# Kernel optimization log

Measured on AMD Instinct MI355X. Metric: run time of the kernel, lower is better.

The kernel has to match this reference:

```python
import jax, jax.numpy as jnp
import numpy as np

B, H, S, D = 2, 16, 4096, 64

def setup_inputs() -> dict:
    key = jax.random.key(0)
    kq, kk, kv = jax.random.split(key, 3)
    Q = jax.random.normal(kq, (B, H, S, D), dtype=jnp.float32)
    K = jax.random.normal(kk, (B, H, S, D), dtype=jnp.float32)
    V = jax.random.normal(kv, (B, H, S, D), dtype=jnp.float32)
    return {"Q": Q, "K": K, "V": V}

def reference(Q, K, V):
    # scores: [B, H, S, S] = Q @ K^T, scaled by 1/sqrt(D) BEFORE softmax
    scale = 1.0 / jnp.sqrt(jnp.asarray(Q.shape[-1], Q.dtype))
    scores = jnp.einsum('bhqd,bhkd->bhqk', Q, K) * scale
    attn = jax.nn.softmax(scores, axis=-1)
    # output: [B, H, S, D]
    return jnp.einsum('bhqk,bhkd->bhqd', attn, V)
```

## Files before the change

kernel.cpp:

```cpp
#include <hip/hip_runtime.h>
#include <hip/hip_bf16.h>

namespace {

constexpr int kS  = 4096;
constexpr int kD  = 64;
constexpr int kQB = 256;
constexpr int kKV = 64;
constexpr int kBH = 2 * 16;
constexpr int kNT = kS / kKV;
constexpr int kNWG = (kS / kQB) * kBH;

typedef __attribute__((ext_vector_type(8))) short bf16x8;
typedef __attribute__((ext_vector_type(4))) short s16x4;
typedef __attribute__((ext_vector_type(4))) float f32x4;
typedef unsigned short u16;

constexpr float SCL  = 0.18033688011112042f;
constexpr float BIAS = -8.0f;

__device__ __forceinline__ u16 f2bf(float f) {
  union { __hip_bfloat16 h; u16 u; } c;
  c.h = __float2bfloat16(f);
  return c.u;
}

__device__ __forceinline__ void gload_lds16(const void* g, void* l) {
  __builtin_amdgcn_global_load_lds(
      (const __attribute__((address_space(1))) unsigned int*)g,
      (__attribute__((address_space(3))) unsigned int*)l, 16, 0, 0);
}

__device__ __forceinline__ int vt_idx(int d, int k) {
  const int swz = (((d >> 4) & 3) << 4) ^ ((d & 15) << 2);
  return d * kKV + (k ^ swz);
}

__global__ __launch_bounds__(256)
void cvt2_bf16(const float* __restrict__ K, const float* __restrict__ V,
               u16* __restrict__ dst, int n8) {
  const int i = blockIdx.x * 256 + threadIdx.x;
  if (i >= 2 * n8) return;
  const float* src;
  int j;
  if (i < n8) { src = K; j = i; }
  else        { src = V; j = i - n8; }
  const float4 a = *(const float4*)(src + (size_t)j * 8);
  const float4 b = *(const float4*)(src + (size_t)j * 8 + 4);
  union { u16 us[8]; uint4 q; } p;
  p.us[0] = f2bf(a.x); p.us[1] = f2bf(a.y);
  p.us[2] = f2bf(a.z); p.us[3] = f2bf(a.w);
  p.us[4] = f2bf(b.x); p.us[5] = f2bf(b.y);
  p.us[6] = f2bf(b.z); p.us[7] = f2bf(b.w);
  *(uint4*)(dst + (size_t)i * 8) = p.q;
}

__global__ __launch_bounds__(512)
void attn_fwd_bf16(const float* __restrict__ Qg, const u16* __restrict__ Kb,
                   const u16* __restrict__ Vb, float* __restrict__ Og) {
  __shared__ __align__(16) u16 Klds[2][kKV * kD];
  __shared__ __align__(16) u16 Vt[2][kD * kKV];

  const int tid  = threadIdx.x;
  const int lane = tid & 63;
  const int w    = tid >> 6;
  const int g    = lane >> 4;
  const int lq   = lane & 15;

  const int wg   = (blockIdx.x & 7) * (kNWG / 8) + (blockIdx.x >> 3);
  const int bh   = wg >> 4;
  const int qblk = wg & 15;

  const size_t base = (size_t)bh * kS * kD;
  const int qb = qblk * kQB + w * 32;

  bf16x8 qf[2][2];
#pragma unroll
  for (int st = 0; st < 2; ++st) {
    const float* qp = Qg + base + (size_t)(qb + st * 16 + lq) * kD + 8 * g;
#pragma unroll
    for (int dh = 0; dh < 2; ++dh) {
      const float4 a = *(const float4*)(qp + dh * 32);
      const float4 b = *(const float4*)(qp + dh * 32 + 4);
      bf16x8 f;
      f[0] = (short)f2bf(a.x * SCL); f[1] = (short)f2bf(a.y * SCL);
      f[2] = (short)f2bf(a.z * SCL); f[3] = (short)f2bf(a.w * SCL);
      f[4] = (short)f2bf(b.x * SCL); f[5] = (short)f2bf(b.y * SCL);
      f[6] = (short)f2bf(b.z * SCL); f[7] = (short)f2bf(b.w * SCL);
      qf[st][dh] = f;
    }
  }

  bf16x8 onesf;
#pragma unroll
  for (int i = 0; i < 8; ++i) onesf[i] = (short)0x3F80;

  f32x4 oacc[2][4];
#pragma unroll
  for (int st = 0; st < 2; ++st)
#pragma unroll
    for (int dt = 0; dt < 4; ++dt) oacc[st][dt] = f32x4{0.f, 0.f, 0.f, 0.f};
  f32x4 lacc[2] = {{0.f, 0.f, 0.f, 0.f}, {0.f, 0.f, 0.f, 0.f}};

  const u16* Kh = Kb + base;
  const u16* Vh = Vb + base;

  const int k0 = (tid & 15) * 4;
  const int d0 = ((tid >> 4) & 15) * 4;

  ushort4 vr[4];

  auto stageK = [&](const u16* Ktile, u16* Kbuf) {
    const int wv = w - 4;
#pragma unroll
    for (int p = 0; p < 2; ++p) {
      const int L = wv * 2048 + p * 1024 + lane * 16;
      const int row = L >> 7;
      const int colb = (L & 127) ^ ((row & 7) << 4);
      gload_lds16(Ktile + row * kD + (colb >> 1), Kbuf + (wv * 1024 + p * 512));
    }
  };
  auto loadV = [&](const u16* Vtile) {
#pragma unroll
    for (int i = 0; i < 4; ++i)
      vr[i] = *(const ushort4*)(Vtile + (k0 + i) * kD + d0);
  };
  auto writeVt = [&](u16* Vbuf) {
#pragma unroll
    for (int j = 0; j < 4; ++j) {
      s16x4 col;
      col[0] = (short)vr[0][j]; col[1] = (short)vr[1][j];
      col[2] = (short)vr[2][j]; col[3] = (short)vr[3][j];
      *(s16x4*)&Vbuf[vt_idx(d0 + j, k0)] = col;
    }
  };

  if (w >= 4) {
    stageK(Kh, Klds[0]);
  } else {
    loadV(Vh);
    writeVt(Vt[0]);
  }
  __syncthreads();

  const f32x4 cbias = {BIAS, BIAS, BIAS, BIAS};

  int cur = 0;
  for (int t = 0; t < kNT; ++t) {
    const bool pf = (t + 1 < kNT);
    if (pf) {
      if (w >= 4) stageK(Kh + (size_t)(t + 1) * kKV * kD, Klds[cur ^ 1]);
      else        loadV(Vh + (size_t)(t + 1) * kKV * kD);
    }

    f32x4 s[2][4];
    __builtin_amdgcn_s_setprio(1);
#pragma unroll
    for (int kt = 0; kt < 4; ++kt) {
      const int krow = kt * 16 + lq;
      const char* kbp = (const char*)Klds[cur] + krow * 128;
      const int sw = (krow & 7) << 4;
      const bf16x8 kf0 = *(const bf16x8*)(kbp + ((16 * g) ^ sw));
      const bf16x8 kf1 = *(const bf16x8*)(kbp + ((16 * g + 64) ^ sw));
#pragma unroll
      for (int st = 0; st < 2; ++st) {
        f32x4 acc = __builtin_amdgcn_mfma_f32_16x16x32_bf16(
            kf0, qf[st][0], cbias, 0, 0, 0);
        s[st][kt] = __builtin_amdgcn_mfma_f32_16x16x32_bf16(
            kf1, qf[st][1], acc, 0, 0, 0);
      }
    }
    __builtin_amdgcn_s_setprio(0);

    bf16x8 pfr[2][2];
#pragma unroll
    for (int st = 0; st < 2; ++st) {
#pragma unroll
      for (int kt = 0; kt < 4; ++kt)
#pragma unroll
        for (int rr = 0; rr < 4; ++rr)
          s[st][kt][rr] = __builtin_amdgcn_exp2f(s[st][kt][rr]);
#pragma unroll
      for (int kc = 0; kc < 2; ++kc) {
        bf16x8 f;
#pragma unroll
        for (int i = 0; i < 4; ++i) {
          f[i]     = (short)f2bf(s[st][2 * kc][i]);
          f[4 + i] = (short)f2bf(s[st][2 * kc + 1][i]);
        }
        pfr[st][kc] = f;
      }
    }

    __builtin_amdgcn_s_setprio(1);
#pragma unroll
    for (int st = 0; st < 2; ++st)
#pragma unroll
      for (int kc = 0; kc < 2; ++kc)
        lacc[st] = __builtin_amdgcn_mfma_f32_16x16x32_bf16(
            onesf, pfr[st][kc], lacc[st], 0, 0, 0);
#pragma unroll
    for (int dt = 0; dt < 4; ++dt) {
      const int d = dt * 16 + lq;
#pragma unroll
      for (int kc = 0; kc < 2; ++kc) {
        const s16x4 lo = *(const s16x4*)&Vt[cur][vt_idx(d, kc * 32 + 4 * g)];
        const s16x4 hi = *(const s16x4*)&Vt[cur][vt_idx(d, kc * 32 + 16 + 4 * g)];
        const bf16x8 vf =
            __builtin_shufflevector(lo, hi, 0, 1, 2, 3, 4, 5, 6, 7);
#pragma unroll
        for (int st = 0; st < 2; ++st)
          oacc[st][dt] = __builtin_amdgcn_mfma_f32_16x16x32_bf16(
              vf, pfr[st][kc], oacc[st][dt], 0, 0, 0);
      }
    }
    __builtin_amdgcn_s_setprio(0);

    if (pf && w < 4) writeVt(Vt[cur ^ 1]);
    __syncthreads();
    cur ^= 1;
  }

#pragma unroll
  for (int st = 0; st < 2; ++st) {
    const float inv = 1.0f / lacc[st][0];
    float* op = Og + base + (size_t)(qb + st * 16 + lq) * kD;
#pragma unroll
    for (int dt = 0; dt < 4; ++dt) {
      f32x4 o = oacc[st][dt];
      o *= inv;
      *(f32x4*)(op + dt * 16 + 4 * g) = o;
    }
  }
}

__global__ __launch_bounds__(256)
void attn_fwd_f32(const float* __restrict__ Qg, const float* __restrict__ Kg,
                  const float* __restrict__ Vg, float* __restrict__ Og) {
  __shared__ __align__(16) u16 Klds[kKV * kD];
  __shared__ __align__(16) u16 Vts[kD * kKV];

  const int tid  = threadIdx.x;
  const int lane = tid & 63;
  const int w    = tid >> 6;
  const int g    = lane >> 4;
  const int lq   = lane & 15;

  const size_t base = (size_t)blockIdx.y * kS * kD;
  const int qb = blockIdx.x * 128 + w * 32;

  bf16x8 qf[2][2];
#pragma unroll
  for (int st = 0; st < 2; ++st) {
    const float* qp = Qg + base + (size_t)(qb + st * 16 + lq) * kD + 8 * g;
#pragma unroll
    for (int dh = 0; dh < 2; ++dh) {
      const float4 a = *(const float4*)(qp + dh * 32);
      const float4 b = *(const float4*)(qp + dh * 32 + 4);
      bf16x8 f;
      f[0] = (short)f2bf(a.x * SCL); f[1] = (short)f2bf(a.y * SCL);
      f[2] = (short)f2bf(a.z * SCL); f[3] = (short)f2bf(a.w * SCL);
      f[4] = (short)f2bf(b.x * SCL); f[5] = (short)f2bf(b.y * SCL);
      f[6] = (short)f2bf(b.z * SCL); f[7] = (short)f2bf(b.w * SCL);
      qf[st][dh] = f;
    }
  }

  f32x4 oacc[2][4];
#pragma unroll
  for (int st = 0; st < 2; ++st)
#pragma unroll
    for (int dt = 0; dt < 4; ++dt) oacc[st][dt] = f32x4{0.f, 0.f, 0.f, 0.f};
  float m_run[2] = {-__builtin_inff(), -__builtin_inff()};
  float l_run[2] = {0.0f, 0.0f};

  const int r  = tid >> 2;
  const int c0 = (tid & 3) * 16;

  for (int kv = 0; kv < kS; kv += kKV) {
    __syncthreads();
    {
      const float* kp = Kg + base + (size_t)(kv + r) * kD + c0;
      const float* vp = Vg + base + (size_t)(kv + r) * kD + c0;
      float4 kq[4], vq[4];
#pragma unroll
      for (int j = 0; j < 4; ++j) kq[j] = *(const float4*)(kp + 4 * j);
#pragma unroll
      for (int j = 0; j < 4; ++j) vq[j] = *(const float4*)(vp + 4 * j);
      const float* kfp = (const float*)kq;
      const float* vfp = (const float*)vq;
      union { u16 us[8]; uint4 q; } p0, p1;
#pragma unroll
      for (int j = 0; j < 8; ++j) {
        p0.us[j] = f2bf(kfp[j]);
        p1.us[j] = f2bf(kfp[8 + j]);
      }
      char* kb = (char*)Klds + r * 128;
      const int sw = (r & 7) << 4;
      *(uint4*)(kb + ((c0 * 2) ^ sw))      = p0.q;
      *(uint4*)(kb + ((c0 * 2 + 16) ^ sw)) = p1.q;
#pragma unroll
      for (int j = 0; j < 16; ++j) Vts[vt_idx(c0 + j, r)] = f2bf(vfp[j]);
    }
    __syncthreads();

    f32x4 s[2][4];
#pragma unroll
    for (int kt = 0; kt < 4; ++kt) {
      const int krow = kt * 16 + lq;
      const char* kb = (const char*)Klds + krow * 128;
      const int sw = (krow & 7) << 4;
      const bf16x8 kf0 = *(const bf16x8*)(kb + ((16 * g) ^ sw));
      const bf16x8 kf1 = *(const bf16x8*)(kb + ((16 * g + 64) ^ sw));
#pragma unroll
      for (int st = 0; st < 2; ++st) {
        f32x4 acc = __builtin_amdgcn_mfma_f32_16x16x32_bf16(
            kf0, qf[st][0], f32x4{0.f, 0.f, 0.f, 0.f}, 0, 0, 0);
        s[st][kt] = __builtin_amdgcn_mfma_f32_16x16x32_bf16(
            kf1, qf[st][1], acc, 0, 0, 0);
      }
    }

    bf16x8 pfr[2][2];
#pragma unroll
    for (int st = 0; st < 2; ++st) {
      float mx = s[st][0][0];
#pragma unroll
      for (int kt = 0; kt < 4; ++kt)
#pragma unroll
        for (int rr = 0; rr < 4; ++rr) mx = fmaxf(mx, s[st][kt][rr]);
      mx = fmaxf(mx, __shfl_xor(mx, 16));
      mx = fmaxf(mx, __shfl_xor(mx, 32));
      const float mnew  = fmaxf(m_run[st], mx);
      const float alpha = exp2f(m_run[st] - mnew);
      m_run[st] = mnew;
      float ps = 0.0f;
#pragma unroll
      for (int kt = 0; kt < 4; ++kt)
#pragma unroll
        for (int rr = 0; rr < 4; ++rr) {
          const float e = exp2f(s[st][kt][rr] - mnew);
          s[st][kt][rr] = e;
          ps += e;
        }
      ps += __shfl_xor(ps, 16);
      ps += __shfl_xor(ps, 32);
      l_run[st] = l_run[st] * alpha + ps;
#pragma unroll
      for (int dt = 0; dt < 4; ++dt) oacc[st][dt] *= alpha;
#pragma unroll
      for (int kc = 0; kc < 2; ++kc) {
        bf16x8 f;
#pragma unroll
        for (int i = 0; i < 4; ++i) {
          f[i]     = (short)f2bf(s[st][2 * kc][i]);
          f[4 + i] = (short)f2bf(s[st][2 * kc + 1][i]);
        }
        pfr[st][kc] = f;
      }
    }

#pragma unroll
    for (int dt = 0; dt < 4; ++dt) {
      const int d = dt * 16 + lq;
#pragma unroll
      for (int kc = 0; kc < 2; ++kc) {
        const s16x4 lo = *(const s16x4*)&Vts[vt_idx(d, kc * 32 + 4 * g)];
        const s16x4 hi = *(const s16x4*)&Vts[vt_idx(d, kc * 32 + 16 + 4 * g)];
        const bf16x8 vf =
            __builtin_shufflevector(lo, hi, 0, 1, 2, 3, 4, 5, 6, 7);
#pragma unroll
        for (int st = 0; st < 2; ++st)
          oacc[st][dt] = __builtin_amdgcn_mfma_f32_16x16x32_bf16(
              vf, pfr[st][kc], oacc[st][dt], 0, 0, 0);
      }
    }
  }

#pragma unroll
  for (int st = 0; st < 2; ++st) {
    const float inv = 1.0f / l_run[st];
    float* op = Og + base + (size_t)(qb + st * 16 + lq) * kD;
#pragma unroll
    for (int dt = 0; dt < 4; ++dt) {
      f32x4 o = oacc[st][dt];
      o *= inv;
      *(f32x4*)(op + dt * 16 + 4 * g) = o;
    }
  }
}

}

extern "C" void kernel_launch(void* const* d_in, const int* in_sizes, int n_in,
                              void* d_out, int out_size, void* d_ws, size_t ws_size,
                              hipStream_t stream) {
  const float* Q = (const float*)d_in[0];
  const float* K = (const float*)d_in[1];
  const float* V = (const float*)d_in[2];
  float* O = (float*)d_out;
  const int n = in_sizes[0];
  const size_t tbytes = (size_t)n * 2;

  if (ws_size >= 2 * tbytes) {
    u16* Kb = (u16*)d_ws;
    u16* Vb = Kb + n;
    const int n8 = n / 8;
    const int cblk = (2 * n8 + 255) / 256;
    cvt2_bf16<<<cblk, 256, 0, stream>>>(K, V, Kb, n8);
    attn_fwd_bf16<<<dim3(kNWG), 512, 0, stream>>>(Q, Kb, Vb, O);
  } else {
    dim3 grid(kS / 128, kBH);
    attn_fwd_f32<<<grid, 256, 0, stream>>>(Q, K, V, O);
  }
}
```

Measured before the change: 162.3 us.

## Pre-transpose V into swizzled tile layout in convert kernel, stage via direct LDS loads

```diff
diff --git a/kernel.cpp b/kernel.cpp
--- a/kernel.cpp
+++ b/kernel.cpp
@@ -10,6 +10,7 @@
 constexpr int kBH = 2 * 16;
 constexpr int kNT = kS / kKV;
 constexpr int kNWG = (kS / kQB) * kBH;
+constexpr int kTileE = kKV * kD;
 
 typedef __attribute__((ext_vector_type(8))) short bf16x8;
 typedef __attribute__((ext_vector_type(4))) short s16x4;
@@ -37,29 +38,58 @@
 }
 
 __global__ __launch_bounds__(256)
-void cvt2_bf16(const float* __restrict__ K, const float* __restrict__ V,
-               u16* __restrict__ dst, int n8) {
-  const int i = blockIdx.x * 256 + threadIdx.x;
-  if (i >= 2 * n8) return;
-  const float* src;
-  int j;
-  if (i < n8) { src = K; j = i; }
-  else        { src = V; j = i - n8; }
-  const float4 a = *(const float4*)(src + (size_t)j * 8);
-  const float4 b = *(const float4*)(src + (size_t)j * 8 + 4);
-  union { u16 us[8]; uint4 q; } p;
-  p.us[0] = f2bf(a.x); p.us[1] = f2bf(a.y);
-  p.us[2] = f2bf(a.z); p.us[3] = f2bf(a.w);
-  p.us[4] = f2bf(b.x); p.us[5] = f2bf(b.y);
-  p.us[6] = f2bf(b.z); p.us[7] = f2bf(b.w);
-  *(uint4*)(dst + (size_t)i * 8) = p.q;
+void cvt_k_vt(const float* __restrict__ K, const float* __restrict__ V,
+              u16* __restrict__ Kb, u16* __restrict__ Vtg, int n16, int nKBlk) {
+  __shared__ __align__(16) u16 Vts[kTileE];
+  const int t = threadIdx.x;
+  if ((int)blockIdx.x < nKBlk) {
+    const int i = blockIdx.x * 256 + t;
+    if (i >= n16) return;
+#pragma unroll
+    for (int h = 0; h < 2; ++h) {
+      const size_t e = (size_t)i * 16 + h * 8;
+      const float4 a = *(const float4*)(K + e);
+      const float4 b = *(const float4*)(K + e + 4);
+      union { u16 us[8]; uint4 q; } p;
+      p.us[0] = f2bf(a.x); p.us[1] = f2bf(a.y);
+      p.us[2] = f2bf(a.z); p.us[3] = f2bf(a.w);
+      p.us[4] = f2bf(b.x); p.us[5] = f2bf(b.y);
+      p.us[6] = f2bf(b.z); p.us[7] = f2bf(b.w);
+      *(uint4*)(Kb + e) = p.q;
+    }
+    return;
+  }
+  const int v    = blockIdx.x - nKBlk;
+  const int head = v >> 6;
+  const int tile = v & 63;
+  const float* Vt0 = V + (size_t)head * kS * kD + (size_t)tile * kKV * kD;
+  const int k0 = (t & 15) * 4;
+  const int d0 = (t >> 4) * 4;
+  float4 r[4];
+#pragma unroll
+  for (int i = 0; i < 4; ++i)
+    r[i] = *(const float4*)(Vt0 + (k0 + i) * kD + d0);
+#pragma unroll
+  for (int j = 0; j < 4; ++j) {
+    const float c0 = (&r[0].x)[j], c1 = (&r[1].x)[j];
+    const float c2 = (&r[2].x)[j], c3 = (&r[3].x)[j];
+    s16x4 col;
+    col[0] = (short)f2bf(c0); col[1] = (short)f2bf(c1);
+    col[2] = (short)f2bf(c2); col[3] = (short)f2bf(c3);
+    *(s16x4*)&Vts[vt_idx(d0 + j, k0)] = col;
+  }
+  __syncthreads();
+  u16* dst = Vtg + (size_t)(head * 64 + tile) * kTileE;
+#pragma unroll
+  for (int p = 0; p < 2; ++p)
+    *(uint4*)(dst + p * 2048 + t * 8) = *(const uint4*)&Vts[p * 2048 + t * 8];
 }
 
 __global__ __launch_bounds__(512)
 void attn_fwd_bf16(const float* __restrict__ Qg, const u16* __restrict__ Kb,
-                   const u16* __restrict__ Vb, float* __restrict__ Og) {
-  __shared__ __align__(16) u16 Klds[2][kKV * kD];
-  __shared__ __align__(16) u16 Vt[2][kD * kKV];
+                   const u16* __restrict__ Vtg, float* __restrict__ Og) {
+  __shared__ __align__(16) u16 Klds[2][kTileE];
+  __shared__ __align__(16) u16 Vt[2][kTileE];
 
   const int tid  = threadIdx.x;
   const int lane = tid & 63;
@@ -102,13 +132,8 @@
     for (int dt = 0; dt < 4; ++dt) oacc[st][dt] = f32x4{0.f, 0.f, 0.f, 0.f};
   f32x4 lacc[2] = {{0.f, 0.f, 0.f, 0.f}, {0.f, 0.f, 0.f, 0.f}};
 
-  const u16* Kh = Kb + base;
-  const u16* Vh = Vb + base;
-
-  const int k0 = (tid & 15) * 4;
-  const int d0 = ((tid >> 4) & 15) * 4;
-
-  ushort4 vr[4];
+  const u16* Kh  = Kb + base;
+  const u16* Vth = Vtg + base;
 
   auto stageK = [&](const u16* Ktile, u16* Kbuf) {
     const int wv = w - 4;
@@ -120,27 +145,15 @@
       gload_lds16(Ktile + row * kD + (colb >> 1), Kbuf + (wv * 1024 + p * 512));
     }
   };
-  auto loadV = [&](const u16* Vtile) {
-#pragma unroll
-    for (int i = 0; i < 4; ++i)
-      vr[i] = *(const ushort4*)(Vtile + (k0 + i) * kD + d0);
+  auto stageV = [&](const u16* Vtile, u16* Vbuf) {
+#pragma unroll
+    for (int p = 0; p < 2; ++p)
+      gload_lds16(Vtile + w * 1024 + p * 512 + lane * 8,
+                  Vbuf + (w * 1024 + p * 512));
   };
-  auto writeVt = [&](u16* Vbuf) {
-#pragma unroll
-    for (int j = 0; j < 4; ++j) {
-      s16x4 col;
-      col[0] = (short)vr[0][j]; col[1] = (short)vr[1][j];
-      col[2] = (short)vr[2][j]; col[3] = (short)vr[3][j];
-      *(s16x4*)&Vbuf[vt_idx(d0 + j, k0)] = col;
-    }
-  };
-
-  if (w >= 4) {
-    stageK(Kh, Klds[0]);
-  } else {
-    loadV(Vh);
-    writeVt(Vt[0]);
-  }
+
+  if (w >= 4) stageK(Kh, Klds[0]);
+  else        stageV(Vth, Vt[0]);
   __syncthreads();
 
   const f32x4 cbias = {BIAS, BIAS, BIAS, BIAS};
@@ -149,8 +162,8 @@
   for (int t = 0; t < kNT; ++t) {
     const bool pf = (t + 1 < kNT);
     if (pf) {
-      if (w >= 4) stageK(Kh + (size_t)(t + 1) * kKV * kD, Klds[cur ^ 1]);
-      else        loadV(Vh + (size_t)(t + 1) * kKV * kD);
+      if (w >= 4) stageK(Kh + (size_t)(t + 1) * kTileE, Klds[cur ^ 1]);
+      else        stageV(Vth + (size_t)(t + 1) * kTileE, Vt[cur ^ 1]);
     }
 
     f32x4 s[2][4];
@@ -216,7 +229,6 @@
     }
     __builtin_amdgcn_s_setprio(0);
 
-    if (pf && w < 4) writeVt(Vt[cur ^ 1]);
     __syncthreads();
     cur ^= 1;
   }
@@ -403,12 +415,13 @@
   const size_t tbytes = (size_t)n * 2;
 
   if (ws_size >= 2 * tbytes) {
-    u16* Kb = (u16*)d_ws;
-    u16* Vb = Kb + n;
-    const int n8 = n / 8;
-    const int cblk = (2 * n8 + 255) / 256;
-    cvt2_bf16<<<cblk, 256, 0, stream>>>(K, V, Kb, n8);
-    attn_fwd_bf16<<<dim3(kNWG), 512, 0, stream>>>(Q, Kb, Vb, O);
+    u16* Kb  = (u16*)d_ws;
+    u16* Vtg = Kb + n;
+    const int n16  = n / 16;
+    const int nKBlk = (n16 + 255) / 256;
+    const int nVBlk = kBH * (kS / kKV);
+    cvt_k_vt<<<nKBlk + nVBlk, 256, 0, stream>>>(K, V, Kb, Vtg, n16, nKBlk);
+    attn_fwd_bf16<<<dim3(kNWG), 512, 0, stream>>>(Q, Kb, Vtg, O);
   } else {
     dim3 grid(kS / 128, kBH);
     attn_fwd_f32<<<grid, 256, 0, stream>>>(Q, K, V, O);
```

New measurement: 169.1 us. +4.2%, slower.
